# Kernel optimization log

Hardware: AMD Instinct MI355X
Metric: run time of the kernel (lower is better)

The kernel has to match this reference:

```python
import jax, jax.numpy as jnp
import numpy as np

B, S, D = 4, 4096, 256


def setup_inputs() -> dict:
    key = jax.random.key(0)
    ks = jax.random.split(key, 7)
    s = 1.0 / np.sqrt(D)
    return {
        "x": jax.random.normal(ks[0], (B, S, D), dtype=jnp.float32),
        "Wq": jax.random.uniform(ks[1], (D, D), jnp.float32, -s, s),
        "bq": jax.random.uniform(ks[2], (D,), jnp.float32, -s, s),
        "Wk": jax.random.uniform(ks[3], (D, D), jnp.float32, -s, s),
        "bk": jax.random.uniform(ks[4], (D,), jnp.float32, -s, s),
        "Wv": jax.random.uniform(ks[5], (D, D), jnp.float32, -s, s),
        "bv": jax.random.uniform(ks[6], (D,), jnp.float32, -s, s),
    }


def reference(x, Wq, bq, Wk, bk, Wv, bv):
    # nn.Linear: y = x @ W.T + b
    Q = jnp.einsum("bsd,ed->bse", x, Wq) + bq
    K = jnp.einsum("bsd,ed->bse", x, Wk) + bk
    V = jnp.einsum("bsd,ed->bse", x, Wv) + bv
    dk = Q.shape[-1]
    scores = jnp.einsum("bqd,bkd->bqk", Q, K) / jnp.sqrt(jnp.float32(dk))
    # NOTE: original applies softmax over dim=1 (the query axis), not -1.
    attn = jax.nn.softmax(scores, axis=1)
    out = jnp.einsum("bqk,bkd->bqd", attn, V)
    return out
```

## Files before the change

### kernel.cpp

```cpp
#include <hip/hip_runtime.h>

typedef short bf16x8 __attribute__((ext_vector_type(8)));
typedef float f32x4 __attribute__((ext_vector_type(4)));
typedef unsigned short u16;

#define S_LEN 4096
#define D_DIM 256
#define NROW  16384

__device__ __forceinline__ u16 f2bf(float f) {
    union { float f; unsigned u; } v; v.f = f;
    unsigned r = v.u + 0x7FFFu + ((v.u >> 16) & 1u);
    return (u16)(r >> 16);
}

__device__ __forceinline__ size_t fr_qk(int t, int kk) {
    return (size_t)t * 4096 + kk * 512;
}
__device__ __forceinline__ size_t fr_v(int p, int dt, int kk2) {
    return (size_t)p * 16384 + (dt * 2 + kk2) * 512;
}

__device__ __forceinline__ void gll16(const u16* g, u16* l) {
    __builtin_amdgcn_global_load_lds(
        (const __attribute__((address_space(1))) unsigned int*)g,
        (__attribute__((address_space(3))) unsigned int*)l, 16, 0, 0);
}

__global__ __launch_bounds__(256) void wconv(
    const float* __restrict__ Wq, const float* __restrict__ Wk,
    const float* __restrict__ Wv, u16* __restrict__ Wf)
{
    int i = blockIdx.x * 256 + threadIdx.x;
    int m = i >> 13;
    int idx = i & 8191;
    int ocol = idx >> 5;
    int d0 = (idx & 31) * 8;
    const float* s = (m == 0 ? Wq : (m == 1 ? Wk : Wv)) + ocol * 256 + d0;
    float4 v0 = *reinterpret_cast<const float4*>(s);
    float4 v1 = *reinterpret_cast<const float4*>(s + 4);
    union { ushort4 h[2]; int4 q; } t;
    t.h[0] = make_ushort4(f2bf(v0.x), f2bf(v0.y), f2bf(v0.z), f2bf(v0.w));
    t.h[1] = make_ushort4(f2bf(v1.x), f2bf(v1.y), f2bf(v1.z), f2bf(v1.w));
    size_t off = (size_t)m * 65536 + fr_qk(ocol >> 4, d0 >> 5)
               + ((d0 >> 3) & 3) * 128 + (ocol & 15) * 8;
    *reinterpret_cast<int4*>(Wf + off) = t.q;
}

__global__ __launch_bounds__(256) void qkv_proj(
    const float* __restrict__ x, const u16* __restrict__ Wf,
    const float* __restrict__ bq, const float* __restrict__ bk,
    const float* __restrict__ bv,
    u16* __restrict__ Qf, u16* __restrict__ Kf, u16* __restrict__ Vf)
{
    __shared__ u16 xs[32][264];
    const int tid = threadIdx.x;
    const int r0 = blockIdx.x * 32;

    #pragma unroll
    for (int i = 0; i < 8; ++i) {
        int c = i * 256 + tid;
        int row = c >> 6, c4 = c & 63;
        float4 v = reinterpret_cast<const float4*>(x + (size_t)(r0 + row) * D_DIM)[c4];
        *reinterpret_cast<ushort4*>(&xs[row][c4 * 4]) =
            make_ushort4(f2bf(v.x), f2bf(v.y), f2bf(v.z), f2bf(v.w));
    }
    __syncthreads();

    const int w = tid >> 6, l = tid & 63, lr = l & 15, lg = l >> 4;
    const int c0 = w * 64;

    bf16x8 a[2][8];
    #pragma unroll
    for (int qs = 0; qs < 2; ++qs)
        #pragma unroll
        for (int kk = 0; kk < 8; ++kk)
            a[qs][kk] = *reinterpret_cast<const bf16x8*>(&xs[qs * 16 + lr][kk * 32 + lg * 8]);

    const float* Bs[3] = {bq, bk, bv};

    #pragma unroll
    for (int m = 0; m < 3; ++m) {
        const u16* Wm = Wf + (size_t)m * 65536;
        f32x4 acc[2][4] = {};
        #pragma unroll
        for (int kk = 0; kk < 8; ++kk) {
            #pragma unroll
            for (int cf = 0; cf < 4; ++cf) {
                bf16x8 wfr = *reinterpret_cast<const bf16x8*>(
                    Wm + fr_qk(w * 4 + cf, kk) + l * 8);
                acc[0][cf] = __builtin_amdgcn_mfma_f32_16x16x32_bf16(a[0][kk], wfr, acc[0][cf], 0, 0, 0);
                acc[1][cf] = __builtin_amdgcn_mfma_f32_16x16x32_bf16(a[1][kk], wfr, acc[1][cf], 0, 0, 0);
            }
        }
        if (m < 2) {
            u16* outp = (m == 0) ? Qf : Kf;
            int t = r0 >> 4;
            #pragma unroll
            for (int qs = 0; qs < 2; ++qs) {
                #pragma unroll
                for (int cf = 0; cf < 4; ++cf) {
                    int col = c0 + cf * 16 + lr;
                    float bias = Bs[m][col];
                    size_t base = fr_qk(t + qs, col >> 5) + ((col >> 3) & 3) * 128 + (col & 7);
                    #pragma unroll
                    for (int r = 0; r < 4; ++r)
                        outp[base + (lg * 4 + r) * 8] = f2bf(acc[qs][cf][r] + bias);
                }
            }
        } else {
            int p  = (r0 >> 12) * 64 + ((r0 & 4095) >> 6);
            int kb = r0 & 63;
            #pragma unroll
            for (int qs = 0; qs < 2; ++qs) {
                #pragma unroll
                for (int cf = 0; cf < 4; ++cf) {
                    int d = c0 + cf * 16 + lr;
                    float bias = bv[d];
                    #pragma unroll
                    for (int r = 0; r < 4; ++r) {
                        int key = kb + qs * 16 + lg * 4 + r;
                        size_t off = fr_v(p, d >> 4, key >> 5)
                                   + ((key >> 3) & 3) * 128 + (d & 15) * 8 + (key & 7);
                        Vf[off] = f2bf(acc[qs][cf][r] + bias);
                    }
                }
            }
        }
    }
}

__global__ __launch_bounds__(256, 4) void col_denom(
    const u16* __restrict__ Qf, const u16* __restrict__ Kf, float* __restrict__ Zp)
{
    __shared__ __align__(16) u16 Qls[2][8192];
    const int tid = threadIdx.x, blk = blockIdx.x;
    const int xcd = blk & 7;
    const int b = xcd >> 1, qhalf = xcd & 1;
    const int idx = blk >> 3;
    const int w = tid >> 6, l = tid & 63, lr = l & 15, lg = l >> 4;
    const int k0 = idx * 64;

    const int tkw = b * 256 + idx * 4 + w;
    bf16x8 kreg[8];
    #pragma unroll
    for (int kk = 0; kk < 8; ++kk)
        kreg[kk] = *reinterpret_cast<const bf16x8*>(Kf + fr_qk(tkw, kk) + l * 8);

    #define STAGE_Q(qt_, nb_) do { \
        const u16* g_ = Qf + ((size_t)(b * 256 + (qt_) * 2)) * 4096 + (w * 4) * 512 + l * 8; \
        u16* d_ = &Qls[nb_][(w * 4) * 512]; \
        _Pragma("unroll") \
        for (int f_ = 0; f_ < 4; ++f_) gll16(g_ + f_ * 512, d_ + f_ * 512); \
    } while (0)

    const int qt0 = qhalf * 64;
    STAGE_Q(qt0, 0);
    __syncthreads();

    float Z[4] = {};
    const float SC = 0.0625f;

    for (int it = 0; it < 64; ++it) {
        const int cur = it & 1;
        if (it < 63) STAGE_Q(qt0 + it + 1, cur ^ 1);

        f32x4 acc[2] = {};
        #pragma unroll
        for (int kk = 0; kk < 8; ++kk) {
            #pragma unroll
            for (int qf = 0; qf < 2; ++qf) {
                bf16x8 qfr = *reinterpret_cast<const bf16x8*>(
                    &Qls[cur][(qf * 8 + kk) * 512 + l * 8]);
                acc[qf] = __builtin_amdgcn_mfma_f32_16x16x32_bf16(kreg[kk], qfr, acc[qf], 0, 0, 0);
            }
        }
        #pragma unroll
        for (int qf = 0; qf < 2; ++qf)
            #pragma unroll
            for (int r = 0; r < 4; ++r)
                Z[r] += __expf(acc[qf][r] * SC);
        __syncthreads();
    }

    #pragma unroll
    for (int r = 0; r < 4; ++r) {
        float z = Z[r];
        z += __shfl_xor(z, 1);
        z += __shfl_xor(z, 2);
        z += __shfl_xor(z, 4);
        z += __shfl_xor(z, 8);
        if (lr == 0)
            Zp[qhalf * NROW + b * S_LEN + k0 + w * 16 + lg * 4 + r] = z;
    }
    #undef STAGE_Q
}

__global__ __launch_bounds__(256) void zlog(
    const float* __restrict__ Zp, float* __restrict__ LZ)
{
    int i = blockIdx.x * 256 + threadIdx.x;
    LZ[i] = logf(Zp[i] + Zp[NROW + i]);
}

__global__ __launch_bounds__(256, 2) void attn_out(
    const u16* __restrict__ Qf, const u16* __restrict__ Kf, const u16* __restrict__ Vf,
    const float* __restrict__ LZ, float* __restrict__ out)
{
    __shared__ __align__(16) u16 Kls[2][8192];
    __shared__ __align__(16) u16 Vls[2][8192];
    __shared__ __align__(16) u16 ps[4][640];

    const int tid = threadIdx.x, blk = blockIdx.x;
    const int xcd = blk & 7;
    const int b = xcd >> 1, khalf = xcd & 1;
    const int idx = blk >> 3;
    const int w = tid >> 6, l = tid & 63, lr = l & 15, lg = l >> 4;
    const int q0 = idx * 64 + w * 16;
    const int base_tk = b * 256;

    const int tq = base_tk + (q0 >> 4);
    bf16x8 qreg[8];
    #pragma unroll
    for (int kk = 0; kk < 8; ++kk)
        qreg[kk] = *reinterpret_cast<const bf16x8*>(Qf + fr_qk(tq, kk) + l * 8);

    #define STAGE_KV(kt_, nb_) do { \
        if (w < 2) { \
            const u16* g_ = Kf + ((size_t)(base_tk + (kt_) * 2)) * 4096 + (w * 8) * 512 + l * 8; \
            u16* d_ = &Kls[nb_][(w * 8) * 512]; \
            _Pragma("unroll") \
            for (int f_ = 0; f_ < 8; ++f_) gll16(g_ + f_ * 512, d_ + f_ * 512); \
        } else { \
            const size_t vb_ = ((size_t)(b * 64 + ((kt_) >> 1))) * 16384 + ((kt_) & 1) * 512; \
            const int dt0_ = (w - 2) * 8; \
            _Pragma("unroll") \
            for (int f_ = 0; f_ < 8; ++f_) \
                gll16(Vf + vb_ + (size_t)(dt0_ + f_) * 1024 + l * 8, &Vls[nb_][(dt0_ + f_) * 512]); \
        } \
    } while (0)

    const int kt0 = khalf * 64;
    STAGE_KV(kt0, 0);
    __syncthreads();

    f32x4 oacc[16] = {};
    const float SC = 0.0625f;

    for (int it = 0; it < 64; ++it) {
        const int kt = kt0 + it;
        const int cur = it & 1;
        if (it < 63) STAGE_KV(kt + 1, cur ^ 1);

        float Lv0 = LZ[b * S_LEN + kt * 32 + lr];
        float Lv1 = LZ[b * S_LEN + kt * 32 + 16 + lr];

        f32x4 sacc[2] = {};
        #pragma unroll
        for (int kk = 0; kk < 8; ++kk) {
            #pragma unroll
            for (int cf = 0; cf < 2; ++cf) {
                bf16x8 kfr = *reinterpret_cast<const bf16x8*>(
                    &Kls[cur][(cf * 8 + kk) * 512 + l * 8]);
                sacc[cf] = __builtin_amdgcn_mfma_f32_16x16x32_bf16(qreg[kk], kfr, sacc[cf], 0, 0, 0);
            }
        }
        #pragma unroll
        for (int cf = 0; cf < 2; ++cf) {
            float Lv = cf ? Lv1 : Lv0;
            #pragma unroll
            for (int r = 0; r < 4; ++r) {
                float p = __expf(fmaf(sacc[cf][r], SC, -Lv));
                ps[w][(lg * 4 + r) * 40 + cf * 16 + lr] = f2bf(p);
            }
        }
        bf16x8 af = *reinterpret_cast<const bf16x8*>(&ps[w][lr * 40 + lg * 8]);
        #pragma unroll
        for (int dt = 0; dt < 16; ++dt) {
            bf16x8 vfr = *reinterpret_cast<const bf16x8*>(&Vls[cur][dt * 512 + l * 8]);
            oacc[dt] = __builtin_amdgcn_mfma_f32_16x16x32_bf16(af, vfr, oacc[dt], 0, 0, 0);
        }
        __syncthreads();
    }

    #pragma unroll
    for (int dt = 0; dt < 16; ++dt) {
        #pragma unroll
        for (int r = 0; r < 4; ++r) {
            int row = q0 + lg * 4 + r;
            unsafeAtomicAdd(&out[((size_t)(b * S_LEN + row)) * D_DIM + dt * 16 + lr],
                            oacc[dt][r]);
        }
    }
    #undef STAGE_KV
}

extern "C" void kernel_launch(void* const* d_in, const int* in_sizes, int n_in,
                              void* d_out, int out_size, void* d_ws, size_t ws_size,
                              hipStream_t stream) {
    const float* x  = (const float*)d_in[0];
    const float* Wq = (const float*)d_in[1];
    const float* bq = (const float*)d_in[2];
    const float* Wk = (const float*)d_in[3];
    const float* bk = (const float*)d_in[4];
    const float* Wv = (const float*)d_in[5];
    const float* bv = (const float*)d_in[6];
    float* out = (float*)d_out;

    u16* Qf = (u16*)d_ws;
    u16* Kf = Qf + (size_t)NROW * D_DIM;
    u16* Vf = Kf + (size_t)NROW * D_DIM;
    u16* Wf = Vf + (size_t)NROW * D_DIM;
    float* Zp = (float*)(Wf + 196608);
    float* LZ = Zp + 2 * NROW;

    hipMemsetAsync(out, 0, (size_t)NROW * D_DIM * sizeof(float), stream);

    wconv<<<96, 256, 0, stream>>>(Wq, Wk, Wv, Wf);
    qkv_proj<<<NROW / 32, 256, 0, stream>>>(x, Wf, bq, bk, bv, Qf, Kf, Vf);
    col_denom<<<512, 256, 0, stream>>>(Qf, Kf, Zp);
    zlog<<<NROW / 256, 256, 0, stream>>>(Zp, LZ);
    attn_out<<<512, 256, 0, stream>>>(Qf, Kf, Vf, LZ, out);
}
```

Measured before the change: 189.1 us.

## Double per-wave tile size in col_denom and attn_out, split reduction four ways

Each wave in col_denom now handles 32 keys instead of 16, and each wave in attn_out handles 32 queries instead of 16. Every shared-memory fragment of Q, or of K and V, loaded from LDS therefore feeds twice as many MFMAs, cutting LDS traffic per unit of work. To keep the grid at 512 blocks, the reduction dimension is split into four quarters instead of two. This needs four partial denominators summed in zlog and more atomic adds per output row. It also raises register pressure (col_denom's launch bounds drop from 4 to 2 blocks per SM) and doubles the ps buffer.

```diff
diff --git a/kernel.cpp b/kernel.cpp
--- a/kernel.cpp
+++ b/kernel.cpp
@@ -130,22 +130,26 @@
     }
 }
 
-__global__ __launch_bounds__(256, 4) void col_denom(
+__global__ __launch_bounds__(256, 2) void col_denom(
     const u16* __restrict__ Qf, const u16* __restrict__ Kf, float* __restrict__ Zp)
 {
     __shared__ __align__(16) u16 Qls[2][8192];
     const int tid = threadIdx.x, blk = blockIdx.x;
-    const int xcd = blk & 7;
-    const int b = xcd >> 1, qhalf = xcd & 1;
-    const int idx = blk >> 3;
+    const int xcd = blk & 7, sub = blk >> 3;
+    const int b  = xcd >> 1;
+    const int qq = ((xcd & 1) << 1) | (sub & 1);
+    const int ktile = sub >> 1;
     const int w = tid >> 6, l = tid & 63, lr = l & 15, lg = l >> 4;
-    const int k0 = idx * 64;
-
-    const int tkw = b * 256 + idx * 4 + w;
-    bf16x8 kreg[8];
-    #pragma unroll
-    for (int kk = 0; kk < 8; ++kk)
-        kreg[kk] = *reinterpret_cast<const bf16x8*>(Kf + fr_qk(tkw, kk) + l * 8);
+    const int k0 = ktile * 128;
+
+    bf16x8 kreg[2][8];
+    #pragma unroll
+    for (int ks = 0; ks < 2; ++ks) {
+        const int tk = b * 256 + (k0 >> 4) + w * 2 + ks;
+        #pragma unroll
+        for (int kk = 0; kk < 8; ++kk)
+            kreg[ks][kk] = *reinterpret_cast<const bf16x8*>(Kf + fr_qk(tk, kk) + l * 8);
+    }
 
     #define STAGE_Q(qt_, nb_) do { \
         const u16* g_ = Qf + ((size_t)(b * 256 + (qt_) * 2)) * 4096 + (w * 4) * 512 + l * 8; \
@@ -154,44 +158,50 @@
         for (int f_ = 0; f_ < 4; ++f_) gll16(g_ + f_ * 512, d_ + f_ * 512); \
     } while (0)
 
-    const int qt0 = qhalf * 64;
+    const int qt0 = qq * 32;
     STAGE_Q(qt0, 0);
     __syncthreads();
 
-    float Z[4] = {};
+    float Z[2][4] = {};
     const float SC = 0.0625f;
 
-    for (int it = 0; it < 64; ++it) {
+    for (int it = 0; it < 32; ++it) {
         const int cur = it & 1;
-        if (it < 63) STAGE_Q(qt0 + it + 1, cur ^ 1);
-
-        f32x4 acc[2] = {};
+        if (it < 31) STAGE_Q(qt0 + it + 1, cur ^ 1);
+
+        f32x4 acc[2][2] = {};
         #pragma unroll
         for (int kk = 0; kk < 8; ++kk) {
             #pragma unroll
             for (int qf = 0; qf < 2; ++qf) {
                 bf16x8 qfr = *reinterpret_cast<const bf16x8*>(
                     &Qls[cur][(qf * 8 + kk) * 512 + l * 8]);
-                acc[qf] = __builtin_amdgcn_mfma_f32_16x16x32_bf16(kreg[kk], qfr, acc[qf], 0, 0, 0);
-            }
-        }
-        #pragma unroll
-        for (int qf = 0; qf < 2; ++qf)
-            #pragma unroll
-            for (int r = 0; r < 4; ++r)
-                Z[r] += __expf(acc[qf][r] * SC);
+                acc[0][qf] = __builtin_amdgcn_mfma_f32_16x16x32_bf16(kreg[0][kk], qfr, acc[0][qf], 0, 0, 0);
+                acc[1][qf] = __builtin_amdgcn_mfma_f32_16x16x32_bf16(kreg[1][kk], qfr, acc[1][qf], 0, 0, 0);
+            }
+        }
+        #pragma unroll
+        for (int ks = 0; ks < 2; ++ks)
+            #pragma unroll
+            for (int qf = 0; qf < 2; ++qf)
+                #pragma unroll
+                for (int r = 0; r < 4; ++r)
+                    Z[ks][r] += __expf(acc[ks][qf][r] * SC);
         __syncthreads();
     }
 
     #pragma unroll
-    for (int r = 0; r < 4; ++r) {
-        float z = Z[r];
-        z += __shfl_xor(z, 1);
-        z += __shfl_xor(z, 2);
-        z += __shfl_xor(z, 4);
-        z += __shfl_xor(z, 8);
-        if (lr == 0)
-            Zp[qhalf * NROW + b * S_LEN + k0 + w * 16 + lg * 4 + r] = z;
+    for (int ks = 0; ks < 2; ++ks) {
+        #pragma unroll
+        for (int r = 0; r < 4; ++r) {
+            float z = Z[ks][r];
+            z += __shfl_xor(z, 1);
+            z += __shfl_xor(z, 2);
+            z += __shfl_xor(z, 4);
+            z += __shfl_xor(z, 8);
+            if (lr == 0)
+                Zp[qq * NROW + b * S_LEN + k0 + w * 32 + ks * 16 + lg * 4 + r] = z;
+        }
     }
     #undef STAGE_Q
 }
@@ -200,7 +210,7 @@
     const float* __restrict__ Zp, float* __restrict__ LZ)
 {
     int i = blockIdx.x * 256 + threadIdx.x;
-    LZ[i] = logf(Zp[i] + Zp[NROW + i]);
+    LZ[i] = logf(((Zp[i] + Zp[NROW + i]) + Zp[2 * NROW + i]) + Zp[3 * NROW + i]);
 }
 
 __global__ __launch_bounds__(256, 2) void attn_out(
@@ -209,21 +219,25 @@
 {
     __shared__ __align__(16) u16 Kls[2][8192];
     __shared__ __align__(16) u16 Vls[2][8192];
-    __shared__ __align__(16) u16 ps[4][640];
+    __shared__ __align__(16) u16 ps[4][1280];
 
     const int tid = threadIdx.x, blk = blockIdx.x;
-    const int xcd = blk & 7;
-    const int b = xcd >> 1, khalf = xcd & 1;
-    const int idx = blk >> 3;
+    const int xcd = blk & 7, sub = blk >> 3;
+    const int b  = xcd >> 1;
+    const int kq = ((xcd & 1) << 1) | (sub & 1);
+    const int qtile = sub >> 1;
     const int w = tid >> 6, l = tid & 63, lr = l & 15, lg = l >> 4;
-    const int q0 = idx * 64 + w * 16;
+    const int q0 = qtile * 128 + w * 32;
     const int base_tk = b * 256;
 
-    const int tq = base_tk + (q0 >> 4);
-    bf16x8 qreg[8];
-    #pragma unroll
-    for (int kk = 0; kk < 8; ++kk)
-        qreg[kk] = *reinterpret_cast<const bf16x8*>(Qf + fr_qk(tq, kk) + l * 8);
+    bf16x8 qreg[2][8];
+    #pragma unroll
+    for (int qs = 0; qs < 2; ++qs) {
+        const int tq = base_tk + ((q0 + qs * 16) >> 4);
+        #pragma unroll
+        for (int kk = 0; kk < 8; ++kk)
+            qreg[qs][kk] = *reinterpret_cast<const bf16x8*>(Qf + fr_qk(tq, kk) + l * 8);
+    }
 
     #define STAGE_KV(kt_, nb_) do { \
         if (w < 2) { \
@@ -240,56 +254,59 @@
         } \
     } while (0)
 
-    const int kt0 = khalf * 64;
+    const int kt0 = kq * 32;
     STAGE_KV(kt0, 0);
     __syncthreads();
 
-    f32x4 oacc[16] = {};
+    f32x4 oacc[2][16] = {};
     const float SC = 0.0625f;
 
-    for (int it = 0; it < 64; ++it) {
+    for (int it = 0; it < 32; ++it) {
         const int kt = kt0 + it;
         const int cur = it & 1;
-        if (it < 63) STAGE_KV(kt + 1, cur ^ 1);
-
-        float Lv0 = LZ[b * S_LEN + kt * 32 + lr];
-        float Lv1 = LZ[b * S_LEN + kt * 32 + 16 + lr];
-
-        f32x4 sacc[2] = {};
-        #pragma unroll
-        for (int kk = 0; kk < 8; ++kk) {
-            #pragma unroll
-            for (int cf = 0; cf < 2; ++cf) {
+        if (it < 31) STAGE_KV(kt + 1, cur ^ 1);
+
+        #pragma unroll
+        for (int cf = 0; cf < 2; ++cf) {
+            float Lv = LZ[b * S_LEN + kt * 32 + cf * 16 + lr];
+            f32x4 sacc[2] = {};
+            #pragma unroll
+            for (int kk = 0; kk < 8; ++kk) {
                 bf16x8 kfr = *reinterpret_cast<const bf16x8*>(
                     &Kls[cur][(cf * 8 + kk) * 512 + l * 8]);
-                sacc[cf] = __builtin_amdgcn_mfma_f32_16x16x32_bf16(qreg[kk], kfr, sacc[cf], 0, 0, 0);
-            }
-        }
-        #pragma unroll
-        for (int cf = 0; cf < 2; ++cf) {
-            float Lv = cf ? Lv1 : Lv0;
-            #pragma unroll
-            for (int r = 0; r < 4; ++r) {
-                float p = __expf(fmaf(sacc[cf][r], SC, -Lv));
-                ps[w][(lg * 4 + r) * 40 + cf * 16 + lr] = f2bf(p);
-            }
-        }
-        bf16x8 af = *reinterpret_cast<const bf16x8*>(&ps[w][lr * 40 + lg * 8]);
+                sacc[0] = __builtin_amdgcn_mfma_f32_16x16x32_bf16(qreg[0][kk], kfr, sacc[0], 0, 0, 0);
+                sacc[1] = __builtin_amdgcn_mfma_f32_16x16x32_bf16(qreg[1][kk], kfr, sacc[1], 0, 0, 0);
+            }
+            #pragma unroll
+            for (int qs = 0; qs < 2; ++qs) {
+                #pragma unroll
+                for (int r = 0; r < 4; ++r) {
+                    float p = __expf(fmaf(sacc[qs][r], SC, -Lv));
+                    ps[w][(qs * 16 + lg * 4 + r) * 40 + cf * 16 + lr] = f2bf(p);
+                }
+            }
+        }
+        bf16x8 af0 = *reinterpret_cast<const bf16x8*>(&ps[w][lr * 40 + lg * 8]);
+        bf16x8 af1 = *reinterpret_cast<const bf16x8*>(&ps[w][(16 + lr) * 40 + lg * 8]);
         #pragma unroll
         for (int dt = 0; dt < 16; ++dt) {
             bf16x8 vfr = *reinterpret_cast<const bf16x8*>(&Vls[cur][dt * 512 + l * 8]);
-            oacc[dt] = __builtin_amdgcn_mfma_f32_16x16x32_bf16(af, vfr, oacc[dt], 0, 0, 0);
+            oacc[0][dt] = __builtin_amdgcn_mfma_f32_16x16x32_bf16(af0, vfr, oacc[0][dt], 0, 0, 0);
+            oacc[1][dt] = __builtin_amdgcn_mfma_f32_16x16x32_bf16(af1, vfr, oacc[1][dt], 0, 0, 0);
         }
         __syncthreads();
     }
 
     #pragma unroll
-    for (int dt = 0; dt < 16; ++dt) {
-        #pragma unroll
-        for (int r = 0; r < 4; ++r) {
-            int row = q0 + lg * 4 + r;
-            unsafeAtomicAdd(&out[((size_t)(b * S_LEN + row)) * D_DIM + dt * 16 + lr],
-                            oacc[dt][r]);
+    for (int qs = 0; qs < 2; ++qs) {
+        #pragma unroll
+        for (int dt = 0; dt < 16; ++dt) {
+            #pragma unroll
+            for (int r = 0; r < 4; ++r) {
+                int row = q0 + qs * 16 + lg * 4 + r;
+                unsafeAtomicAdd(&out[((size_t)(b * S_LEN + row)) * D_DIM + dt * 16 + lr],
+                                oacc[qs][dt][r]);
+            }
         }
     }
     #undef STAGE_KV
@@ -312,7 +329,7 @@
     u16* Vf = Kf + (size_t)NROW * D_DIM;
     u16* Wf = Vf + (size_t)NROW * D_DIM;
     float* Zp = (float*)(Wf + 196608);
-    float* LZ = Zp + 2 * NROW;
+    float* LZ = Zp + 4 * NROW;
 
     hipMemsetAsync(out, 0, (size_t)NROW * D_DIM * sizeof(float), stream);
 
```

Measured after the change: 186.0 us. About the same (-1.6%).
